# Performance work log

Measured on AMD Instinct MI355X. Metric: run time of the kernel, lower is better.

Reference implementation:

```python
import jax, jax.numpy as jnp
import numpy as np

B, N, D, H = 8, 1024, 768, 12
HD = D // H
SCALE = HD ** -0.5

def setup_inputs() -> dict:
    key = jax.random.key(0)
    k1, k2, k3, k4 = jax.random.split(key, 4)
    x = jax.random.normal(k1, (B, N, D), dtype=jnp.float32)
    weight = jax.random.uniform(k2, (B, N), dtype=jnp.float32)
    W_qkv = jax.random.normal(k3, (D, 3 * D), dtype=jnp.float32) * (D ** -0.5)
    W_msa = jax.random.normal(k4, (D, D), dtype=jnp.float32) * (D ** -0.5)
    b_msa = jnp.zeros((D,), dtype=jnp.float32)
    return {"x": x, "weight": weight, "W_qkv": W_qkv, "W_msa": W_msa, "b_msa": b_msa}

def reference(x, weight, W_qkv, W_msa, b_msa):
    # QKV projection (no bias), then elementwise per-token gate
    qkv = jnp.einsum('bnd,de->bne', x, W_qkv)          # [B,N,3D]
    qkv = weight[:, :, None] * qkv
    qkv = qkv.reshape(B, N, 3, H, HD).transpose(2, 0, 3, 1, 4)  # [3,B,H,N,hd]
    q, k, v = qkv[0], qkv[1], qkv[2]
    A = jnp.einsum('bhnd,bhmd->bhnm', q, k) * SCALE    # [B,H,N,N]
    A = jax.nn.softmax(A, axis=-1)
    out = jnp.einsum('bhnm,bhmd->bhnd', A, v)          # [B,H,N,hd]
    out = out.transpose(0, 2, 1, 3).reshape(B, N, D)
    return jnp.einsum('bnd,de->bne', out, W_msa) + b_msa
```

## Files before the change

kernel.cpp:

```cpp
#include <hip/hip_runtime.h>
#include <hip/hip_bf16.h>


typedef __attribute__((ext_vector_type(8))) short bf8;
typedef __attribute__((ext_vector_type(4))) float f4;

#define QSCALE 0.1803368801111204f

static __device__ __forceinline__ short bf16_of(float f) {
    union { float f; unsigned u; } a; a.f = f;
    unsigned r = a.u + 0x7FFFu + ((a.u >> 16) & 1u);
    return (short)(r >> 16);
}

static __device__ __forceinline__ unsigned bfpk(float lo, float hi) {
    float2 t; t.x = lo; t.y = hi;
    __hip_bfloat162 b = __float22bfloat162_rn(t);
    union { __hip_bfloat162 b; unsigned u; } c; c.b = b;
    return c.u;
}

static __device__ __forceinline__ void async16(const short* g, short* l) {
    __builtin_amdgcn_global_load_lds(
        (const __attribute__((address_space(1))) void*)g,
        (__attribute__((address_space(3))) void*)l, 16, 0, 0);
}

__global__ __launch_bounds__(256) void k_cvt(const float* __restrict__ src,
                                             const float* __restrict__ gate,
                                             short* __restrict__ dst, int n8) {
    int i = blockIdx.x * 256 + threadIdx.x;
    if (i >= n8) return;
    const float g = gate[i / 96];
    const f4* sp = (const f4*)src;
    f4 a = sp[2 * i], b = sp[2 * i + 1];
    union { bf8 v; short h[8]; } o;
    o.h[0] = bf16_of(a[0] * g); o.h[1] = bf16_of(a[1] * g);
    o.h[2] = bf16_of(a[2] * g); o.h[3] = bf16_of(a[3] * g);
    o.h[4] = bf16_of(b[0] * g); o.h[5] = bf16_of(b[1] * g);
    o.h[6] = bf16_of(b[2] * g); o.h[7] = bf16_of(b[3] * g);
    ((bf8*)dst)[i] = o.v;
}

__global__ __launch_bounds__(256) void k_transpose(const float* __restrict__ w,
                                                   short* __restrict__ wt,
                                                   int K, int E) {
    __shared__ short t[64][65];
    const int k0 = blockIdx.y * 64, e0 = blockIdx.x * 64;
    const int tid = threadIdx.x;
#pragma unroll
    for (int p = 0; p < 16; ++p) {
        int idx = p * 256 + tid;
        int r = idx >> 6, c = idx & 63;
        t[r][c] = bf16_of(w[(k0 + r) * E + e0 + c]);
    }
    __syncthreads();
#pragma unroll
    for (int p = 0; p < 16; ++p) {
        int idx = p * 256 + tid;
        int r = idx >> 6, c = idx & 63;
        wt[(e0 + r) * K + k0 + c] = t[c][r];
    }
}

static __device__ __forceinline__ void gemm128(const short* __restrict__ gA,
                                               const short* __restrict__ gB,
                                               short* smem,
                                               f4 acc[4][4]) {
    const int tid = threadIdx.x, lane = tid & 63;
    const int l16 = lane & 15, quad = lane >> 4, rx = l16 & 7;
    const int wm = (tid >> 6) & 1, wn = tid >> 7;

    auto stage = [&](short* S, int k0) {
#pragma unroll
        for (int c = 0; c < 4; ++c) {
            int p = c * 256 + tid;
            int row = p >> 3, slot = p & 7;
            int gc = slot ^ (row & 7);
            async16(gA + row * 768 + k0 + gc * 8, S + p * 8);
            async16(gB + row * 768 + k0 + gc * 8, S + 8192 + p * 8);
        }
    };

    stage(smem, 0);
    for (int it = 0; it < 12; ++it) {
        __builtin_amdgcn_s_waitcnt(0);
        __syncthreads();
        short* Sc = smem + (it & 1) * 16384;
        if (it + 1 < 12) stage(smem + ((it + 1) & 1) * 16384, (it + 1) * 64);
        const short* As = Sc;
        const short* Bs = Sc + 8192;
#pragma unroll
        for (int ks = 0; ks < 2; ++ks) {
            bf8 af[4], bfr[4];
#pragma unroll
            for (int mt = 0; mt < 4; ++mt)
                af[mt] = *(const bf8*)(As + (wm * 64 + mt * 16 + l16) * 64 +
                                       (((ks * 4 + quad) ^ rx) * 8));
#pragma unroll
            for (int nt = 0; nt < 4; ++nt)
                bfr[nt] = *(const bf8*)(Bs + (wn * 64 + nt * 16 + l16) * 64 +
                                        (((ks * 4 + quad) ^ rx) * 8));
#pragma unroll
            for (int mt = 0; mt < 4; ++mt)
#pragma unroll
                for (int nt = 0; nt < 4; ++nt)
                    acc[mt][nt] = __builtin_amdgcn_mfma_f32_16x16x32_bf16(
                        af[mt], bfr[nt], acc[mt][nt], 0, 0, 0);
        }
    }
    __syncthreads();
}

__global__ __launch_bounds__(512, 2) void k_gemm_qkv(
        const short* __restrict__ xb, const short* __restrict__ wtq,
        short* __restrict__ qb, short* __restrict__ kb, short* __restrict__ vt) {
    __shared__ short lds[69632];
    const int tid = threadIdx.x, lane = tid & 63;
    const int l16 = lane & 15, quad = lane >> 4, rx = l16 & 7;
    const int wv = tid >> 6, wm = wv >> 1, wn = wv & 1;

    const int wg = blockIdx.x;
    const int swz = (wg & 7) * 32 + (wg >> 3);
    const int mI = swz >> 3, nI = swz & 7;
    const int m0 = mI * 256, n0 = nI * 288;

    const short* gA = xb + m0 * 768;
    const short* gB = wtq + n0 * 768;

    auto stageA = [&](int buf, int half, int k0) {
        short* dst = lds + buf * 34816 + half * 8192;
        const short* src = gA + half * 98304 + k0;
#pragma unroll
        for (int j = 0; j < 2; ++j) {
            int p = j * 512 + tid;
            int row = p >> 3;
            int gc = (p & 7) ^ (row & 7);
            async16(src + row * 768 + gc * 8, dst + p * 8);
        }
    };
    auto stageB = [&](int buf, int half, int k0) {
        short* dst = lds + buf * 34816 + 16384 + half * 9216;
        const short* src = gB + half * 110592 + k0;
#pragma unroll
        for (int j = 0; j < 2; ++j) {
            int p = j * 512 + tid;
            int row = p >> 3;
            int gc = (p & 7) ^ (row & 7);
            async16(src + row * 768 + gc * 8, dst + p * 8);
        }
        if (tid < 128) {
            int p = 1024 + tid;
            int row = p >> 3;
            int gc = (p & 7) ^ (row & 7);
            async16(src + row * 768 + gc * 8, dst + p * 8);
        }
    };

    f4 z = {0.f, 0.f, 0.f, 0.f};
    f4 acc[4][9];
#pragma unroll
    for (int mf = 0; mf < 4; ++mf)
#pragma unroll
        for (int nf = 0; nf < 9; ++nf) acc[mf][nf] = z;

    stageA(0, 0, 0); stageA(0, 1, 0);
    stageB(0, 0, 0); stageB(0, 1, 0);
    stageB(1, 0, 64);
    if (wv < 2) asm volatile("s_waitcnt vmcnt(3)" ::: "memory");
    else        asm volatile("s_waitcnt vmcnt(2)" ::: "memory");
    __builtin_amdgcn_s_barrier();

#pragma unroll 2
    for (int t = 0; t < 12; ++t) {
        const short* Ab = lds + (t & 1) * 34816;
        const short* Bb = Ab + 16384;
        auto rdA = [&](int mf, int ks) {
            return *(const bf8*)(Ab + (wm * 64 + mf * 16 + l16) * 64 +
                                 (((ks * 4 + quad) ^ rx) << 3));
        };
        auto rdB = [&](int nf, int ks) {
            return *(const bf8*)(Bb + (wn * 144 + nf * 16 + l16) * 64 +
                                 (((ks * 4 + quad) ^ rx) << 3));
        };
        bf8 af[4][2], bfr[9][2];

#pragma unroll
        for (int mf = 0; mf < 2; ++mf) { af[mf][0] = rdA(mf, 0); af[mf][1] = rdA(mf, 1); }
#pragma unroll
        for (int nf = 0; nf < 5; ++nf) { bfr[nf][0] = rdB(nf, 0); bfr[nf][1] = rdB(nf, 1); }
        if (t < 11) stageB((t + 1) & 1, 1, (t + 1) * 64);
        __builtin_amdgcn_s_barrier();
        __builtin_amdgcn_s_setprio(1);
#pragma unroll
        for (int mf = 0; mf < 2; ++mf)
#pragma unroll
            for (int nf = 0; nf < 5; ++nf) {
                acc[mf][nf] = __builtin_amdgcn_mfma_f32_16x16x32_bf16(
                    af[mf][0], bfr[nf][0], acc[mf][nf], 0, 0, 0);
                acc[mf][nf] = __builtin_amdgcn_mfma_f32_16x16x32_bf16(
                    af[mf][1], bfr[nf][1], acc[mf][nf], 0, 0, 0);
            }
        __builtin_amdgcn_s_setprio(0);
        __builtin_amdgcn_s_barrier();

#pragma unroll
        for (int mf = 2; mf < 4; ++mf) { af[mf][0] = rdA(mf, 0); af[mf][1] = rdA(mf, 1); }
        if (t < 11) stageA((t + 1) & 1, 0, (t + 1) * 64);
        __builtin_amdgcn_s_barrier();
        __builtin_amdgcn_s_setprio(1);
#pragma unroll
        for (int mf = 2; mf < 4; ++mf)
#pragma unroll
            for (int nf = 0; nf < 5; ++nf) {
                acc[mf][nf] = __builtin_amdgcn_mfma_f32_16x16x32_bf16(
                    af[mf][0], bfr[nf][0], acc[mf][nf], 0, 0, 0);
                acc[mf][nf] = __builtin_amdgcn_mfma_f32_16x16x32_bf16(
                    af[mf][1], bfr[nf][1], acc[mf][nf], 0, 0, 0);
            }
        __builtin_amdgcn_s_setprio(0);
        __builtin_amdgcn_s_barrier();

#pragma unroll
        for (int nf = 5; nf < 9; ++nf) { bfr[nf][0] = rdB(nf, 0); bfr[nf][1] = rdB(nf, 1); }
        if (t < 11) stageA((t + 1) & 1, 1, (t + 1) * 64);
        __builtin_amdgcn_s_barrier();
        __builtin_amdgcn_s_setprio(1);
#pragma unroll
        for (int mf = 0; mf < 2; ++mf)
#pragma unroll
            for (int nf = 5; nf < 9; ++nf) {
                acc[mf][nf] = __builtin_amdgcn_mfma_f32_16x16x32_bf16(
                    af[mf][0], bfr[nf][0], acc[mf][nf], 0, 0, 0);
                acc[mf][nf] = __builtin_amdgcn_mfma_f32_16x16x32_bf16(
                    af[mf][1], bfr[nf][1], acc[mf][nf], 0, 0, 0);
            }
        __builtin_amdgcn_s_setprio(0);
        __builtin_amdgcn_s_barrier();

        if (t < 10) stageB(t & 1, 0, (t + 2) * 64);
        __builtin_amdgcn_s_barrier();
        __builtin_amdgcn_s_setprio(1);
#pragma unroll
        for (int mf = 2; mf < 4; ++mf)
#pragma unroll
            for (int nf = 5; nf < 9; ++nf) {
                acc[mf][nf] = __builtin_amdgcn_mfma_f32_16x16x32_bf16(
                    af[mf][0], bfr[nf][0], acc[mf][nf], 0, 0, 0);
                acc[mf][nf] = __builtin_amdgcn_mfma_f32_16x16x32_bf16(
                    af[mf][1], bfr[nf][1], acc[mf][nf], 0, 0, 0);
            }
        __builtin_amdgcn_s_setprio(0);
        if (t < 10) {
            if (wv < 2) asm volatile("s_waitcnt vmcnt(3)" ::: "memory");
            else        asm volatile("s_waitcnt vmcnt(2)" ::: "memory");
        } else if (t == 10) {
            asm volatile("s_waitcnt vmcnt(0)" ::: "memory");
        }
        __builtin_amdgcn_s_barrier();
    }

    const int bI = m0 >> 10, nn0 = m0 & 1023;
#pragma unroll
    for (int nf = 0; nf < 9; ++nf) {
        const int ct = n0 + wn * 144 + nf * 16;
        if (ct < 1536) {
            const int which = (ct >= 768) ? 1 : 0;
            const int h = (ct - which * 768) >> 6;
            const int hd = (ct & 63) + l16;
            short* dst = (which ? kb : qb) + ((bI * 12 + h) * 1024) * 64 + hd;
#pragma unroll
            for (int mf = 0; mf < 4; ++mf)
#pragma unroll
                for (int r = 0; r < 4; ++r) {
                    const int nn = nn0 + wm * 64 + mf * 16 + quad * 4 + r;
                    const float val = acc[mf][nf][r];
                    dst[nn * 64] = bf16_of(which ? val : val * QSCALE);
                }
        }
    }
    const int vstart = (n0 >= 1536) ? n0 : 1536;
    const int npass = (n0 + 288 > vstart) ? (n0 + 288 - vstart) / 96 : 0;
    for (int p = 0; p < npass; ++p) {
        __syncthreads();
        const int c0 = vstart + p * 96;
#pragma unroll
        for (int nf = 0; nf < 9; ++nf) {
            const int ct = n0 + wn * 144 + nf * 16;
            if (ct >= c0 && ct < c0 + 96) {
                const int lc = ct - c0 + l16;
#pragma unroll
                for (int mf = 0; mf < 4; ++mf)
#pragma unroll
                    for (int r = 0; r < 4; ++r) {
                        const int rl = wm * 64 + mf * 16 + quad * 4 + r;
                        lds[lc * 264 + rl] = bf16_of(acc[mf][nf][r]);
                    }
            }
        }
        __syncthreads();
        const int vg0 = c0 - 1536;
#pragma unroll
        for (int u = 0; u < 6; ++u) {
            const int idx = u * 512 + tid;
            const int lc = idx >> 5, ck = idx & 31;
            const int vg = vg0 + lc;
            const int h = vg >> 6, hd = vg & 63;
            bf8 vv = *(const bf8*)(lds + lc * 264 + ck * 8);
            *(bf8*)(vt + ((bI * 12 + h) * 64 + hd) * 1024 + nn0 + ck * 8) = vv;
        }
    }
}

__global__ __launch_bounds__(256) void k_gemm_final(
        const short* __restrict__ attn, const short* __restrict__ wtm,
        const float* __restrict__ bias, float* __restrict__ out) {
    __shared__ short smem[32768];
    const int lane = threadIdx.x & 63;
    const int l16 = lane & 15, quad = lane >> 4;
    const int wm = (threadIdx.x >> 6) & 1, wn = threadIdx.x >> 7;
    const int m0 = blockIdx.y * 128, n0 = blockIdx.x * 128;
    f4 z = {0.f, 0.f, 0.f, 0.f};
    f4 acc[4][4] = {{z,z,z,z},{z,z,z,z},{z,z,z,z},{z,z,z,z}};
    gemm128(attn + m0 * 768, wtm + n0 * 768, smem, acc);
#pragma unroll
    for (int mt = 0; mt < 4; ++mt) {
#pragma unroll
        for (int r = 0; r < 4; ++r) {
            const int row = m0 + wm * 64 + mt * 16 + quad * 4 + r;
#pragma unroll
            for (int nt = 0; nt < 4; ++nt) {
                const int e = n0 + wn * 64 + nt * 16 + l16;
                out[row * 768 + e] = acc[mt][nt][r] + bias[e];
            }
        }
    }
}

__global__ __launch_bounds__(512) void k_attn(const short* __restrict__ qb,
                                              const short* __restrict__ kb,
                                              const short* __restrict__ vt,
                                              short* __restrict__ attn) {
    __shared__ short Ks[2][4096];
    __shared__ short Vs[2][4096];
    const int tid = threadIdx.x, wave = tid >> 6, lane = tid & 63;
    const int l16 = lane & 15, quad = lane >> 4;
    const int bh = blockIdx.x;
    const int b = bh / 12, h = bh - b * 12;
    const int m_base = blockIdx.y * 128 + wave * 16;
    const short* qh = qb + bh * 65536;
    const short* kh = kb + bh * 65536;
    const short* vh = vt + bh * 65536;

    const int rA = ((l16 >> 2) << 3) + (l16 & 3);
    const int fK = (((rA >> 3) & 1) << 2) + (rA & 3);
    const int sK = (quad ^ fK) * 8;
    const int oAlo = rA * 64 + sK;
    const int oAhi = rA * 64 + (sK ^ 32);
    const int oBlo = oAlo + 256, oBhi = oAhi + 256;
    const int fV = (((l16 >> 3) & 1) << 2) + (l16 & 3);
    const int oV = l16 * 64 + ((quad ^ fV) * 8);

    const short* qp = qh + (m_base + l16) * 64 + quad * 8;
    bf8 qf0 = *(const bf8*)(qp);
    bf8 qf1 = *(const bf8*)(qp + 32);

    union { bf8 v; short h[8]; } onef;
#pragma unroll
    for (int i = 0; i < 8; ++i) onef.h[i] = (short)0x3F80;

    f4 z = {0.f, 0.f, 0.f, 0.f};
    f4 acc[4] = {z, z, z, z};
    f4 accl = z;

    auto stage = [&](int buf, int j0) {
        int idx = tid;
        int row = idx >> 3;
        int fr = (((row >> 3) & 1) << 2) + (row & 3);
        int gc = (idx & 7) ^ fr;
        async16(kh + (j0 + row) * 64 + gc * 8, Ks[buf] + idx * 8);
        async16(vh + row * 1024 + j0 + gc * 8, Vs[buf] + idx * 8);
    };

    stage(0, 0);
    int cur = 0;
    for (int it = 0; it < 16; ++it) {
        __builtin_amdgcn_s_waitcnt(0);
        __syncthreads();
        if (it + 1 < 16) stage(cur ^ 1, (it + 1) * 64);
        const short* Kc = Ks[cur];
        const short* Vc = Vs[cur];

#pragma unroll
        for (int jj = 0; jj < 64; jj += 32) {
            const short* kjj = Kc + jj * 64;
            bf8 kAlo = *(const bf8*)(kjj + oAlo);
            bf8 kAhi = *(const bf8*)(kjj + oAhi);
            bf8 kBlo = *(const bf8*)(kjj + oBlo);
            bf8 kBhi = *(const bf8*)(kjj + oBhi);

            f4 sA = z, sB = z;
            sA = __builtin_amdgcn_mfma_f32_16x16x32_bf16(kAlo, qf0, sA, 0, 0, 0);
            sA = __builtin_amdgcn_mfma_f32_16x16x32_bf16(kAhi, qf1, sA, 0, 0, 0);
            sB = __builtin_amdgcn_mfma_f32_16x16x32_bf16(kBlo, qf0, sB, 0, 0, 0);
            sB = __builtin_amdgcn_mfma_f32_16x16x32_bf16(kBhi, qf1, sB, 0, 0, 0);
            float a0 = __builtin_amdgcn_exp2f(sA[0]);
            float a1 = __builtin_amdgcn_exp2f(sA[1]);
            float a2 = __builtin_amdgcn_exp2f(sA[2]);
            float a3 = __builtin_amdgcn_exp2f(sA[3]);
            float b0 = __builtin_amdgcn_exp2f(sB[0]);
            float b1 = __builtin_amdgcn_exp2f(sB[1]);
            float b2 = __builtin_amdgcn_exp2f(sB[2]);
            float b3 = __builtin_amdgcn_exp2f(sB[3]);
            union { bf8 v; unsigned u[4]; } p;
            p.u[0] = bfpk(a0, a1); p.u[1] = bfpk(a2, a3);
            p.u[2] = bfpk(b0, b1); p.u[3] = bfpk(b2, b3);
            accl = __builtin_amdgcn_mfma_f32_16x16x32_bf16(
                onef.v, p.v, accl, 0, 0, 0);

#pragma unroll
            for (int dt = 0; dt < 4; ++dt) {
                bf8 vf = *(const bf8*)(Vc + dt * 1024 + (oV ^ (jj ? 32 : 0)));
                acc[dt] = __builtin_amdgcn_mfma_f32_16x16x32_bf16(
                    vf, p.v, acc[dt], 0, 0, 0);
            }
        }
        cur ^= 1;
    }

    const float inv = 1.f / accl[0];
    const int row = (b << 10) + m_base + l16;
    short* op = attn + row * 768 + h * 64 + quad * 4;
#pragma unroll
    for (int dt = 0; dt < 4; ++dt)
#pragma unroll
        for (int r = 0; r < 4; ++r)
            op[dt * 16 + r] = bf16_of(acc[dt][r] * inv);
}

extern "C" void kernel_launch(void* const* d_in, const int* in_sizes, int n_in,
                              void* d_out, int out_size, void* d_ws, size_t ws_size,
                              hipStream_t stream) {
    const float* x    = (const float*)d_in[0];
    const float* gate = (const float*)d_in[1];
    const float* Wqkv = (const float*)d_in[2];
    const float* Wmsa = (const float*)d_in[3];
    const float* bmsa = (const float*)d_in[4];
    float* out = (float*)d_out;

    char* ws = (char*)d_ws;
    short* xb  = (short*)(ws);
    short* wtq = (short*)(ws + 12582912);
    short* wtm = (short*)(ws + 16121856);
    short* qb  = (short*)(ws + 17301504);
    short* kb  = (short*)(ws + 29884416);
    short* vt  = (short*)(ws + 42467328);
    short* attn = xb;

    k_cvt<<<3072, 256, 0, stream>>>(x, gate, xb, 786432);
    k_transpose<<<dim3(36, 12), 256, 0, stream>>>(Wqkv, wtq, 768, 2304);
    k_transpose<<<dim3(12, 12), 256, 0, stream>>>(Wmsa, wtm, 768, 768);
    k_gemm_qkv<<<256, 512, 0, stream>>>(xb, wtq, qb, kb, vt);
    k_attn<<<dim3(96, 8), 512, 0, stream>>>(qb, kb, vt, attn);
    k_gemm_final<<<dim3(6, 64), 256, 0, stream>>>(attn, wtm, bmsa, out);
}
```

Baseline: 186.1 us.

## Fuse prep kernels and give each attention wave two query tiles

The input conversion and both weight-transpose kernels are merged into one launch with block-index dispatch, which removes two kernel launches. The attention kernel now uses 256 threads per block, and each wave processes 32 query rows in two 16-row tiles. Each K and V fragment read from LDS is reused across both tiles, which halves LDS reads per MFMA. The cost is more registers per wave (two accumulator sets) and fewer waves per block, so latency hiding now depends on the occupancy hint of 3 blocks.

```diff
diff --git a/kernel.cpp b/kernel.cpp
--- a/kernel.cpp
+++ b/kernel.cpp
@@ -26,28 +26,9 @@
         (__attribute__((address_space(3))) void*)l, 16, 0, 0);
 }
 
-__global__ __launch_bounds__(256) void k_cvt(const float* __restrict__ src,
-                                             const float* __restrict__ gate,
-                                             short* __restrict__ dst, int n8) {
-    int i = blockIdx.x * 256 + threadIdx.x;
-    if (i >= n8) return;
-    const float g = gate[i / 96];
-    const f4* sp = (const f4*)src;
-    f4 a = sp[2 * i], b = sp[2 * i + 1];
-    union { bf8 v; short h[8]; } o;
-    o.h[0] = bf16_of(a[0] * g); o.h[1] = bf16_of(a[1] * g);
-    o.h[2] = bf16_of(a[2] * g); o.h[3] = bf16_of(a[3] * g);
-    o.h[4] = bf16_of(b[0] * g); o.h[5] = bf16_of(b[1] * g);
-    o.h[6] = bf16_of(b[2] * g); o.h[7] = bf16_of(b[3] * g);
-    ((bf8*)dst)[i] = o.v;
-}
-
-__global__ __launch_bounds__(256) void k_transpose(const float* __restrict__ w,
-                                                   short* __restrict__ wt,
-                                                   int K, int E) {
-    __shared__ short t[64][65];
-    const int k0 = blockIdx.y * 64, e0 = blockIdx.x * 64;
-    const int tid = threadIdx.x;
+static __device__ __forceinline__ void transpose64(
+        const float* __restrict__ w, short* __restrict__ wt,
+        int K, int E, int k0, int e0, int tid, short (*t)[65]) {
 #pragma unroll
     for (int p = 0; p < 16; ++p) {
         int idx = p * 256 + tid;
@@ -60,6 +41,33 @@
         int idx = p * 256 + tid;
         int r = idx >> 6, c = idx & 63;
         wt[(e0 + r) * K + k0 + c] = t[c][r];
+    }
+}
+
+__global__ __launch_bounds__(256) void k_prep(
+        const float* __restrict__ x, const float* __restrict__ gate,
+        short* __restrict__ xb,
+        const float* __restrict__ Wqkv, short* __restrict__ wtq,
+        const float* __restrict__ Wmsa, short* __restrict__ wtm) {
+    __shared__ short t[64][65];
+    const int bid = blockIdx.x, tid = threadIdx.x;
+    if (bid < 3072) {
+        int i = bid * 256 + tid;
+        const float g = gate[i / 96];
+        const f4* sp = (const f4*)x;
+        f4 a = sp[2 * i], b = sp[2 * i + 1];
+        union { bf8 v; short h[8]; } o;
+        o.h[0] = bf16_of(a[0] * g); o.h[1] = bf16_of(a[1] * g);
+        o.h[2] = bf16_of(a[2] * g); o.h[3] = bf16_of(a[3] * g);
+        o.h[4] = bf16_of(b[0] * g); o.h[5] = bf16_of(b[1] * g);
+        o.h[6] = bf16_of(b[2] * g); o.h[7] = bf16_of(b[3] * g);
+        ((bf8*)xb)[i] = o.v;
+    } else if (bid < 3504) {
+        int tt = bid - 3072;
+        transpose64(Wqkv, wtq, 768, 2304, (tt / 36) * 64, (tt % 36) * 64, tid, t);
+    } else {
+        int tt = bid - 3504;
+        transpose64(Wmsa, wtm, 768, 768, (tt / 12) * 64, (tt % 12) * 64, tid, t);
     }
 }
 
@@ -337,17 +345,17 @@
     }
 }
 
-__global__ __launch_bounds__(512) void k_attn(const short* __restrict__ qb,
-                                              const short* __restrict__ kb,
-                                              const short* __restrict__ vt,
-                                              short* __restrict__ attn) {
+__global__ __launch_bounds__(256, 3) void k_attn(const short* __restrict__ qb,
+                                                 const short* __restrict__ kb,
+                                                 const short* __restrict__ vt,
+                                                 short* __restrict__ attn) {
     __shared__ short Ks[2][4096];
     __shared__ short Vs[2][4096];
     const int tid = threadIdx.x, wave = tid >> 6, lane = tid & 63;
     const int l16 = lane & 15, quad = lane >> 4;
     const int bh = blockIdx.x;
     const int b = bh / 12, h = bh - b * 12;
-    const int m_base = blockIdx.y * 128 + wave * 16;
+    const int m_base = blockIdx.y * 128 + wave * 32;
     const short* qh = qb + bh * 65536;
     const short* kh = kb + bh * 65536;
     const short* vh = vt + bh * 65536;
@@ -361,25 +369,32 @@
     const int fV = (((l16 >> 3) & 1) << 2) + (l16 & 3);
     const int oV = l16 * 64 + ((quad ^ fV) * 8);
 
-    const short* qp = qh + (m_base + l16) * 64 + quad * 8;
-    bf8 qf0 = *(const bf8*)(qp);
-    bf8 qf1 = *(const bf8*)(qp + 32);
+    const short* qp0 = qh + (m_base + l16) * 64 + quad * 8;
+    bf8 qf00 = *(const bf8*)(qp0);
+    bf8 qf01 = *(const bf8*)(qp0 + 32);
+    const short* qp1 = qp0 + 16 * 64;
+    bf8 qf10 = *(const bf8*)(qp1);
+    bf8 qf11 = *(const bf8*)(qp1 + 32);
 
     union { bf8 v; short h[8]; } onef;
 #pragma unroll
     for (int i = 0; i < 8; ++i) onef.h[i] = (short)0x3F80;
 
     f4 z = {0.f, 0.f, 0.f, 0.f};
-    f4 acc[4] = {z, z, z, z};
-    f4 accl = z;
+    f4 acc0[4] = {z, z, z, z};
+    f4 acc1[4] = {z, z, z, z};
+    f4 accl0 = z, accl1 = z;
 
     auto stage = [&](int buf, int j0) {
-        int idx = tid;
-        int row = idx >> 3;
-        int fr = (((row >> 3) & 1) << 2) + (row & 3);
-        int gc = (idx & 7) ^ fr;
-        async16(kh + (j0 + row) * 64 + gc * 8, Ks[buf] + idx * 8);
-        async16(vh + row * 1024 + j0 + gc * 8, Vs[buf] + idx * 8);
+#pragma unroll
+        for (int j = 0; j < 2; ++j) {
+            int idx = j * 256 + tid;
+            int row = idx >> 3;
+            int fr = (((row >> 3) & 1) << 2) + (row & 3);
+            int gc = (idx & 7) ^ fr;
+            async16(kh + (j0 + row) * 64 + gc * 8, Ks[buf] + idx * 8);
+            async16(vh + row * 1024 + j0 + gc * 8, Vs[buf] + idx * 8);
+        }
     };
 
     stage(0, 0);
@@ -398,44 +413,75 @@
             bf8 kAhi = *(const bf8*)(kjj + oAhi);
             bf8 kBlo = *(const bf8*)(kjj + oBlo);
             bf8 kBhi = *(const bf8*)(kjj + oBhi);
-
-            f4 sA = z, sB = z;
-            sA = __builtin_amdgcn_mfma_f32_16x16x32_bf16(kAlo, qf0, sA, 0, 0, 0);
-            sA = __builtin_amdgcn_mfma_f32_16x16x32_bf16(kAhi, qf1, sA, 0, 0, 0);
-            sB = __builtin_amdgcn_mfma_f32_16x16x32_bf16(kBlo, qf0, sB, 0, 0, 0);
-            sB = __builtin_amdgcn_mfma_f32_16x16x32_bf16(kBhi, qf1, sB, 0, 0, 0);
-            float a0 = __builtin_amdgcn_exp2f(sA[0]);
-            float a1 = __builtin_amdgcn_exp2f(sA[1]);
-            float a2 = __builtin_amdgcn_exp2f(sA[2]);
-            float a3 = __builtin_amdgcn_exp2f(sA[3]);
-            float b0 = __builtin_amdgcn_exp2f(sB[0]);
-            float b1 = __builtin_amdgcn_exp2f(sB[1]);
-            float b2 = __builtin_amdgcn_exp2f(sB[2]);
-            float b3 = __builtin_amdgcn_exp2f(sB[3]);
-            union { bf8 v; unsigned u[4]; } p;
-            p.u[0] = bfpk(a0, a1); p.u[1] = bfpk(a2, a3);
-            p.u[2] = bfpk(b0, b1); p.u[3] = bfpk(b2, b3);
-            accl = __builtin_amdgcn_mfma_f32_16x16x32_bf16(
-                onef.v, p.v, accl, 0, 0, 0);
-
-#pragma unroll
-            for (int dt = 0; dt < 4; ++dt) {
-                bf8 vf = *(const bf8*)(Vc + dt * 1024 + (oV ^ (jj ? 32 : 0)));
-                acc[dt] = __builtin_amdgcn_mfma_f32_16x16x32_bf16(
-                    vf, p.v, acc[dt], 0, 0, 0);
+            bf8 vf0 = *(const bf8*)(Vc + 0 * 1024 + (oV ^ (jj ? 32 : 0)));
+            bf8 vf1 = *(const bf8*)(Vc + 1 * 1024 + (oV ^ (jj ? 32 : 0)));
+            bf8 vf2 = *(const bf8*)(Vc + 2 * 1024 + (oV ^ (jj ? 32 : 0)));
+            bf8 vf3 = *(const bf8*)(Vc + 3 * 1024 + (oV ^ (jj ? 32 : 0)));
+
+            {
+                f4 sA = z, sB = z;
+                sA = __builtin_amdgcn_mfma_f32_16x16x32_bf16(kAlo, qf00, sA, 0, 0, 0);
+                sA = __builtin_amdgcn_mfma_f32_16x16x32_bf16(kAhi, qf01, sA, 0, 0, 0);
+                sB = __builtin_amdgcn_mfma_f32_16x16x32_bf16(kBlo, qf00, sB, 0, 0, 0);
+                sB = __builtin_amdgcn_mfma_f32_16x16x32_bf16(kBhi, qf01, sB, 0, 0, 0);
+                float a0 = __builtin_amdgcn_exp2f(sA[0]);
+                float a1 = __builtin_amdgcn_exp2f(sA[1]);
+                float a2 = __builtin_amdgcn_exp2f(sA[2]);
+                float a3 = __builtin_amdgcn_exp2f(sA[3]);
+                float b0 = __builtin_amdgcn_exp2f(sB[0]);
+                float b1 = __builtin_amdgcn_exp2f(sB[1]);
+                float b2 = __builtin_amdgcn_exp2f(sB[2]);
+                float b3 = __builtin_amdgcn_exp2f(sB[3]);
+                union { bf8 v; unsigned u[4]; } p;
+                p.u[0] = bfpk(a0, a1); p.u[1] = bfpk(a2, a3);
+                p.u[2] = bfpk(b0, b1); p.u[3] = bfpk(b2, b3);
+                accl0 = __builtin_amdgcn_mfma_f32_16x16x32_bf16(
+                    onef.v, p.v, accl0, 0, 0, 0);
+                acc0[0] = __builtin_amdgcn_mfma_f32_16x16x32_bf16(vf0, p.v, acc0[0], 0, 0, 0);
+                acc0[1] = __builtin_amdgcn_mfma_f32_16x16x32_bf16(vf1, p.v, acc0[1], 0, 0, 0);
+                acc0[2] = __builtin_amdgcn_mfma_f32_16x16x32_bf16(vf2, p.v, acc0[2], 0, 0, 0);
+                acc0[3] = __builtin_amdgcn_mfma_f32_16x16x32_bf16(vf3, p.v, acc0[3], 0, 0, 0);
+            }
+            {
+                f4 sA = z, sB = z;
+                sA = __builtin_amdgcn_mfma_f32_16x16x32_bf16(kAlo, qf10, sA, 0, 0, 0);
+                sA = __builtin_amdgcn_mfma_f32_16x16x32_bf16(kAhi, qf11, sA, 0, 0, 0);
+                sB = __builtin_amdgcn_mfma_f32_16x16x32_bf16(kBlo, qf10, sB, 0, 0, 0);
+                sB = __builtin_amdgcn_mfma_f32_16x16x32_bf16(kBhi, qf11, sB, 0, 0, 0);
+                float a0 = __builtin_amdgcn_exp2f(sA[0]);
+                float a1 = __builtin_amdgcn_exp2f(sA[1]);
+                float a2 = __builtin_amdgcn_exp2f(sA[2]);
+                float a3 = __builtin_amdgcn_exp2f(sA[3]);
+                float b0 = __builtin_amdgcn_exp2f(sB[0]);
+                float b1 = __builtin_amdgcn_exp2f(sB[1]);
+                float b2 = __builtin_amdgcn_exp2f(sB[2]);
+                float b3 = __builtin_amdgcn_exp2f(sB[3]);
+                union { bf8 v; unsigned u[4]; } p;
+                p.u[0] = bfpk(a0, a1); p.u[1] = bfpk(a2, a3);
+                p.u[2] = bfpk(b0, b1); p.u[3] = bfpk(b2, b3);
+                accl1 = __builtin_amdgcn_mfma_f32_16x16x32_bf16(
+                    onef.v, p.v, accl1, 0, 0, 0);
+                acc1[0] = __builtin_amdgcn_mfma_f32_16x16x32_bf16(vf0, p.v, acc1[0], 0, 0, 0);
+                acc1[1] = __builtin_amdgcn_mfma_f32_16x16x32_bf16(vf1, p.v, acc1[1], 0, 0, 0);
+                acc1[2] = __builtin_amdgcn_mfma_f32_16x16x32_bf16(vf2, p.v, acc1[2], 0, 0, 0);
+                acc1[3] = __builtin_amdgcn_mfma_f32_16x16x32_bf16(vf3, p.v, acc1[3], 0, 0, 0);
             }
         }
         cur ^= 1;
     }
 
-    const float inv = 1.f / accl[0];
-    const int row = (b << 10) + m_base + l16;
-    short* op = attn + row * 768 + h * 64 + quad * 4;
+    const float inv0 = 1.f / accl0[0];
+    const float inv1 = 1.f / accl1[0];
+    const int row0 = (b << 10) + m_base + l16;
+    short* op0 = attn + row0 * 768 + h * 64 + quad * 4;
+    short* op1 = op0 + 16 * 768;
 #pragma unroll
     for (int dt = 0; dt < 4; ++dt)
 #pragma unroll
-        for (int r = 0; r < 4; ++r)
-            op[dt * 16 + r] = bf16_of(acc[dt][r] * inv);
+        for (int r = 0; r < 4; ++r) {
+            op0[dt * 16 + r] = bf16_of(acc0[dt][r] * inv0);
+            op1[dt * 16 + r] = bf16_of(acc1[dt][r] * inv1);
+        }
 }
 
 extern "C" void kernel_launch(void* const* d_in, const int* in_sizes, int n_in,
@@ -457,10 +503,8 @@
     short* vt  = (short*)(ws + 42467328);
     short* attn = xb;
 
-    k_cvt<<<3072, 256, 0, stream>>>(x, gate, xb, 786432);
-    k_transpose<<<dim3(36, 12), 256, 0, stream>>>(Wqkv, wtq, 768, 2304);
-    k_transpose<<<dim3(12, 12), 256, 0, stream>>>(Wmsa, wtm, 768, 768);
+    k_prep<<<3648, 256, 0, stream>>>(x, gate, xb, Wqkv, wtq, Wmsa, wtm);
     k_gemm_qkv<<<256, 512, 0, stream>>>(xb, wtq, qb, kb, vt);
-    k_attn<<<dim3(96, 8), 512, 0, stream>>>(qb, kb, vt, attn);
+    k_attn<<<dim3(96, 8), 256, 0, stream>>>(qb, kb, vt, attn);
     k_gemm_final<<<dim3(6, 64), 256, 0, stream>>>(attn, wtm, bmsa, out);
 }
```

After: 175.7 us. 1.06x faster.
